# Kernel optimization log

Measured on AMD Instinct MI355X. Metric: run time of the kernel, lower is better.

Reference implementation:

```python
import jax, jax.numpy as jnp
import numpy as np

N_NODES = 50000


def _gcn_conv(x, W, b, src, dst, norm, n_nodes):
    # x: [N, Fin], W: [Fin, Fout]
    h = x @ W                                   # [N, Fout]
    msg = h[src] * norm[:, None]                # [E+N, Fout] edge messages
    out = jax.ops.segment_sum(msg, dst, num_segments=n_nodes)
    return out + b


def reference(x, edge_index, W1, b1, W2, b2):
    n = x.shape[0]
    # add self-loops (PyG GCNConv default add_self_loops=True)
    loop = jnp.arange(n, dtype=edge_index.dtype)
    src = jnp.concatenate([edge_index[0], loop])
    dst = jnp.concatenate([edge_index[1], loop])
    # symmetric degree normalization: deg over destination with unit weights
    deg = jax.ops.segment_sum(jnp.ones_like(dst, dtype=x.dtype), dst, num_segments=n)
    dinv = jnp.where(deg > 0, jax.lax.rsqrt(deg), 0.0)
    norm = dinv[src] * dinv[dst]                # [E+N]
    h = _gcn_conv(x, W1, b1, src, dst, norm, n)
    h = jax.nn.relu(h)
    out = _gcn_conv(h, W2, b2, src, dst, norm, n)
    return out


def setup_inputs() -> dict:
    key = jax.random.key(0)
    k1, k2, k3, k4 = jax.random.split(key, 4)
    n, e, fin, hid, fout = N_NODES, 800000, 128, 128, 64
    x = jax.random.normal(k1, (n, fin), dtype=jnp.float32)
    edge_index = jax.random.randint(k2, (2, e), 0, n, dtype=jnp.int64)
    # Glorot-ish init for linear weights, zero bias (PyG default)
    W1 = jax.random.normal(k3, (fin, hid), dtype=jnp.float32) / np.sqrt(fin)
    b1 = jnp.zeros((hid,), dtype=jnp.float32)
    W2 = jax.random.normal(k4, (hid, fout), dtype=jnp.float32) / np.sqrt(hid)
    b2 = jnp.zeros((fout,), dtype=jnp.float32)
    return {"x": x, "edge_index": edge_index, "W1": W1, "b1": b1, "W2": W2, "b2": b2}
```

## Files before the change

### kernel.cpp

```cpp
#include <hip/hip_runtime.h>
#include <hip/hip_bf16.h>


constexpr int FIN = 128;
constexpr int HID = 128;
constexpr int FOUT = 64;
constexpr int CAP = 48;
constexpr int OVF_MAX = 196608;

typedef __attribute__((ext_vector_type(8))) short s16x8;
typedef __attribute__((ext_vector_type(4))) float f32x4;

static __device__ __forceinline__ float bf2f(__hip_bfloat16 v) { return __bfloat162float(v); }
static __device__ __forceinline__ float lo2f(unsigned u) { union { unsigned i; float f; } c; c.i = u << 16; return c.f; }
static __device__ __forceinline__ float hi2f(unsigned u) { union { unsigned i; float f; } c; c.i = u & 0xffff0000u; return c.f; }
static __device__ __forceinline__ unsigned short f2bfu(float f) {
    __hip_bfloat16 h = __float2bfloat16(f);
    union { __hip_bfloat16 h; unsigned short u; } c; c.h = h; return c.u;
}
static __device__ __forceinline__ unsigned pack2(float a, float b) {
    return (unsigned)f2bfu(a) | ((unsigned)f2bfu(b) << 16);
}
static __device__ __forceinline__ void acc_add(float* acc, uint4 v) {
    acc[0] += lo2f(v.x); acc[1] += hi2f(v.x);
    acc[2] += lo2f(v.y); acc[3] += hi2f(v.y);
    acc[4] += lo2f(v.z); acc[5] += hi2f(v.z);
    acc[6] += lo2f(v.w); acc[7] += hi2f(v.w);
}

__global__ __launch_bounds__(256) void k_detect(const unsigned* __restrict__ xw,
                                                const int* __restrict__ eiw,
                                                int E, int* __restrict__ flags,
                                                int* __restrict__ cnt, int N) {
    for (long i = (long)blockIdx.x * 256 + threadIdx.x; i <= N; i += (long)gridDim.x * 256)
        cnt[i] = 0;
    if (blockIdx.x != 0) return;
    __shared__ int s_bf16like, s_oddnz;
    if (threadIdx.x == 0) { s_bf16like = 0; s_oddnz = 0; }
    __syncthreads();
    int c = 0;
    for (int i = threadIdx.x; i < 4096; i += 256) {
        unsigned ex = ((xw[i] & 0xffffu) >> 7) & 0xffu;
        if (ex >= 117u && ex <= 130u) c++;
    }
    atomicAdd(&s_bf16like, c);
    int nz = 0;
    for (int i = threadIdx.x; i < 2048; i += 256)
        if (eiw[2 * i + 1] != 0) nz++;
    atomicAdd(&s_oddnz, nz);
    __syncthreads();
    if (threadIdx.x == 0) {
        flags[0] = (s_bf16like < 2048) ? 1 : 0;
        flags[1] = (s_oddnz == 0) ? 1 : 0;
    }
}

__global__ __launch_bounds__(256) void k_build(const int* __restrict__ ei, int E, int N,
                                               int* __restrict__ cnt,
                                               int* __restrict__ slots,
                                               int* __restrict__ ovf,
                                               int* __restrict__ ovfcnt,
                                               const int* __restrict__ flags) {
    long i = (long)blockIdx.x * 256 + threadIdx.x;
    if (i >= E) return;
    int s, d;
    if (flags[1]) {
        s = ((const int2*)ei)[i].x;
        d = ((const int2*)(ei + 2 * (long)E))[i].x;
    } else {
        s = ei[i];
        d = ei[(long)E + i];
    }
    if ((unsigned)s >= (unsigned)N || (unsigned)d >= (unsigned)N) return;
    int pos = atomicAdd(&cnt[d], 1);
    if (pos < CAP) {
        slots[(long)d * CAP + pos] = s;
    } else {
        int op = atomicAdd(ovfcnt, 1);
        if (op < OVF_MAX) { ovf[2 * op] = d; ovf[2 * op + 1] = s; }
    }
}

template<int CT>
__global__ __launch_bounds__(256) void k_gemm(const void* __restrict__ Xp, int x_follows_flag,
                                              const void* __restrict__ Wp,
                                              const int* __restrict__ cnt,
                                              __hip_bfloat16* __restrict__ G,
                                              const int* __restrict__ flags, int N) {
    constexpr int C = CT * 16;
    __shared__ __align__(16) short Wt[C * 136];
    const bool f32m = flags[0] != 0;
    const bool xf32 = (x_follows_flag != 0) && f32m;
    const int tid = threadIdx.x;
    for (int i = tid; i < 128 * C; i += 256) {
        int k = i / C, n = i % C;
        float wv = f32m ? ((const float*)Wp)[(long)k * C + n]
                        : bf2f(((const __hip_bfloat16*)Wp)[(long)k * C + n]);
        Wt[n * 136 + k] = (short)f2bfu(wv);
    }
    __syncthreads();
    const int w = tid >> 6, lane = tid & 63;
    const int m = lane & 15, quad = lane >> 4;
    const int rowA = blockIdx.x * 64 + w * 16 + m;
    const int rowc = rowA < N ? rowA : N - 1;
    s16x8 afr[4];
#pragma unroll
    for (int kc = 0; kc < 4; ++kc) {
        const int k0 = kc * 32 + quad * 8;
        if (!xf32) {
            afr[kc] = *(const s16x8*)((const __hip_bfloat16*)Xp + (long)rowc * 128 + k0);
        } else {
            const float* p = (const float*)Xp + (long)rowc * 128 + k0;
            s16x8 t;
#pragma unroll
            for (int j = 0; j < 8; ++j) t[j] = (short)f2bfu(p[j]);
            afr[kc] = t;
        }
    }
    const int rbase = blockIdx.x * 64 + w * 16 + quad * 4;
    float dv[4];
#pragma unroll
    for (int r = 0; r < 4; ++r) {
        int rr = min(rbase + r, N - 1);
        dv[r] = rsqrtf((float)(cnt[rr] + 1));
    }
#pragma unroll
    for (int ct = 0; ct < CT; ++ct) {
        f32x4 acc = {0.f, 0.f, 0.f, 0.f};
#pragma unroll
        for (int kc = 0; kc < 4; ++kc) {
            s16x8 bfr = *(const s16x8*)&Wt[(ct * 16 + m) * 136 + kc * 32 + quad * 8];
            acc = __builtin_amdgcn_mfma_f32_16x16x32_bf16(afr[kc], bfr, acc, 0, 0, 0);
        }
#pragma unroll
        for (int r = 0; r < 4; ++r) {
            int rr = rbase + r;
            if (rr < N) G[(long)rr * C + ct * 16 + m] = __float2bfloat16(dv[r] * acc[r]);
        }
    }
}

template<int F, int LAYER1>
__global__ __launch_bounds__(256) void k_gather(const __hip_bfloat16* __restrict__ G,
                                                const int* __restrict__ cnt,
                                                const int* __restrict__ slots,
                                                const int* __restrict__ ovf,
                                                const int* __restrict__ ovfcnt,
                                                const void* __restrict__ bias,
                                                void* __restrict__ outp,
                                                const int* __restrict__ flags, int N) {
    constexpr int L = F / 8;
    constexpr int NODES = 256 / L;
    const int tid = threadIdx.x;
    const int grp = tid / L, lane = tid % L;
    const int node = blockIdx.x * NODES + grp;
    if (node >= N) return;
    const int cd = cnt[node];
    const float wself = rsqrtf((float)(cd + 1));
    const int m = cd < CAP ? cd : CAP;
    const int* sl = slots + (long)node * CAP;
    float acc[8] = {0, 0, 0, 0, 0, 0, 0, 0};
    acc_add(acc, ((const uint4*)(G + (long)node * F))[lane]);
    int i = 0;
    for (; i + 3 < m; i += 4) {
        int s0 = sl[i], s1 = sl[i + 1], s2 = sl[i + 2], s3 = sl[i + 3];
        uint4 v0 = ((const uint4*)(G + (long)s0 * F))[lane];
        uint4 v1 = ((const uint4*)(G + (long)s1 * F))[lane];
        uint4 v2 = ((const uint4*)(G + (long)s2 * F))[lane];
        uint4 v3 = ((const uint4*)(G + (long)s3 * F))[lane];
        acc_add(acc, v0); acc_add(acc, v1); acc_add(acc, v2); acc_add(acc, v3);
    }
    for (; i < m; ++i)
        acc_add(acc, ((const uint4*)(G + (long)sl[i] * F))[lane]);
    if (cd > CAP) {
        int oc = *ovfcnt; oc = oc < OVF_MAX ? oc : OVF_MAX;
        for (int j = 0; j < oc; ++j)
            if (ovf[2 * j] == node)
                acc_add(acc, ((const uint4*)(G + (long)ovf[2 * j + 1] * F))[lane]);
    }
    const bool f32m = flags[0] != 0;
    const int c0 = lane * 8;
    float bv[8];
    if (f32m) {
        const float4* bp = (const float4*)((const float*)bias + c0);
        float4 b0 = bp[0], b1 = bp[1];
        bv[0] = b0.x; bv[1] = b0.y; bv[2] = b0.z; bv[3] = b0.w;
        bv[4] = b1.x; bv[5] = b1.y; bv[6] = b1.z; bv[7] = b1.w;
    } else {
        uint4 b = *(const uint4*)((const __hip_bfloat16*)bias + c0);
        bv[0] = lo2f(b.x); bv[1] = hi2f(b.x); bv[2] = lo2f(b.y); bv[3] = hi2f(b.y);
        bv[4] = lo2f(b.z); bv[5] = hi2f(b.z); bv[6] = lo2f(b.w); bv[7] = hi2f(b.w);
    }
    float o[8];
#pragma unroll
    for (int c = 0; c < 8; ++c) {
        float v = wself * acc[c] + bv[c];
        o[c] = (LAYER1 && v < 0.f) ? 0.f : v;
    }
    if (LAYER1 || !f32m) {
        uint4 pv = { pack2(o[0], o[1]), pack2(o[2], o[3]), pack2(o[4], o[5]), pack2(o[6], o[7]) };
        ((uint4*)outp)[(long)node * L + lane] = pv;
    } else {
        float4* op = (float4*)((float*)outp + (long)node * F + c0);
        op[0] = make_float4(o[0], o[1], o[2], o[3]);
        op[1] = make_float4(o[4], o[5], o[6], o[7]);
    }
}

extern "C" void kernel_launch(void* const* d_in, const int* in_sizes, int n_in,
                              void* d_out, int out_size, void* d_ws, size_t ws_size,
                              hipStream_t stream) {
    const void* x  = d_in[0];
    const int*  ei = (const int*)d_in[1];
    const void* W1 = d_in[2];
    const void* b1 = d_in[3];
    const void* W2 = d_in[4];
    const void* b2 = d_in[5];

    const int N = in_sizes[0] / FIN;
    const int E = in_sizes[1] / 2;

    char* ws = (char*)d_ws;
    int*   flags  = (int*)ws;
    int*   cnt    = (int*)(ws + 4096);
    int*   ovfcnt = cnt + N;
    int*   ovf    = (int*)(ws + 524288);
    int*   slots  = (int*)(ws + 2097152);
    __hip_bfloat16* g  = (__hip_bfloat16*)(ws + 11730944);
    __hip_bfloat16* h1 = (__hip_bfloat16*)(ws + 24530944);
    __hip_bfloat16* g2 = (__hip_bfloat16*)(ws + 37330944);

    const int EB = (E + 255) / 256;
    const int GB = (N + 63) / 64;

    k_detect<<<64, 256, 0, stream>>>((const unsigned*)x, ei, E, flags, cnt, N);
    k_build<<<EB, 256, 0, stream>>>(ei, E, N, cnt, slots, ovf, ovfcnt, flags);
    k_gemm<8><<<GB, 256, 0, stream>>>(x, 1, W1, cnt, g, flags, N);
    k_gather<128, 1><<<(N + 15) / 16, 256, 0, stream>>>(g, cnt, slots, ovf, ovfcnt, b1, h1, flags, N);
    k_gemm<4><<<GB, 256, 0, stream>>>(h1, 0, W2, cnt, g2, flags, N);
    k_gather<64, 0><<<(N + 31) / 32, 256, 0, stream>>>(g2, cnt, slots, ovf, ovfcnt, b2, d_out, flags, N);
}
```

Measured before the change: 230.5 us.

## Build adjacency via two-pass bucketed binning in shared memory instead of global atomics

Replaces the single-pass adjacency build, which did one global atomic per edge on per-node counters, with a two-phase binning. First, edges are histogrammed per bucket of 98 destination nodes and scattered into bucket arrays using LDS atomics plus one global atomic per bucket per block. Then each bucket's slot table is assembled in shared memory and written out with coalesced vector stores. A patch kernel handles bucket overflow, and workspace buffers are reused (g2 aliases g, pairs aliases h1). This adds two kernel launches and more scratch traffic, and depends on the bucket capacity assumption holding.

```diff
diff --git a/kernel.cpp b/kernel.cpp
--- a/kernel.cpp
+++ b/kernel.cpp
@@ -6,7 +6,9 @@
 constexpr int HID = 128;
 constexpr int FOUT = 64;
 constexpr int CAP = 48;
-constexpr int OVF_MAX = 196608;
+constexpr int NPB = 98;
+constexpr int BCAP = 3072;
+constexpr int OVF_MAX = 65536;
 
 typedef __attribute__((ext_vector_type(8))) short s16x8;
 typedef __attribute__((ext_vector_type(4))) float f32x4;
@@ -31,10 +33,8 @@
 __global__ __launch_bounds__(256) void k_detect(const unsigned* __restrict__ xw,
                                                 const int* __restrict__ eiw,
                                                 int E, int* __restrict__ flags,
-                                                int* __restrict__ cnt, int N) {
-    for (long i = (long)blockIdx.x * 256 + threadIdx.x; i <= N; i += (long)gridDim.x * 256)
-        cnt[i] = 0;
-    if (blockIdx.x != 0) return;
+                                                int* __restrict__ gcur) {
+    for (int i = threadIdx.x; i < 1026; i += 256) gcur[i] = 0;
     __shared__ int s_bf16like, s_oddnz;
     if (threadIdx.x == 0) { s_bf16like = 0; s_oddnz = 0; }
     __syncthreads();
@@ -55,29 +55,106 @@
     }
 }
 
-__global__ __launch_bounds__(256) void k_build(const int* __restrict__ ei, int E, int N,
+__global__ __launch_bounds__(256) void k_binA(const int* __restrict__ ei, int E, int N,
+                                              int nbuk,
+                                              int* __restrict__ gcur,
+                                              int2* __restrict__ pairs,
+                                              int2* __restrict__ ovfA,
+                                              int* __restrict__ ovfAcnt,
+                                              const int* __restrict__ flags) {
+    __shared__ int hist[1024];
+    __shared__ int gbase[1024];
+    const int tid = threadIdx.x;
+    const long base = (long)blockIdx.x * 4096;
+    const bool i64 = flags[1] != 0;
+    for (int b = tid; b < nbuk; b += 256) hist[b] = 0;
+    __syncthreads();
+    for (int j = 0; j < 16; ++j) {
+        long i = base + j * 256 + tid;
+        if (i >= E) break;
+        int s, d;
+        if (i64) { s = ((const int2*)ei)[i].x; d = ((const int2*)(ei + 2 * (long)E))[i].x; }
+        else     { s = ei[i]; d = ei[(long)E + i]; }
+        if ((unsigned)s >= (unsigned)N || (unsigned)d >= (unsigned)N) continue;
+        atomicAdd(&hist[d / NPB], 1);
+    }
+    __syncthreads();
+    for (int b = tid; b < nbuk; b += 256) {
+        int h = hist[b];
+        gbase[b] = h > 0 ? atomicAdd(&gcur[b], h) : 0;
+        hist[b] = 0;
+    }
+    __syncthreads();
+    for (int j = 0; j < 16; ++j) {
+        long i = base + j * 256 + tid;
+        if (i >= E) break;
+        int s, d;
+        if (i64) { s = ((const int2*)ei)[i].x; d = ((const int2*)(ei + 2 * (long)E))[i].x; }
+        else     { s = ei[i]; d = ei[(long)E + i]; }
+        if ((unsigned)s >= (unsigned)N || (unsigned)d >= (unsigned)N) continue;
+        int b = d / NPB;
+        int p = gbase[b] + atomicAdd(&hist[b], 1);
+        if (p < BCAP) {
+            pairs[(long)b * BCAP + p] = make_int2(d, s);
+        } else {
+            int op = atomicAdd(ovfAcnt, 1);
+            if (op < OVF_MAX) ovfA[op] = make_int2(d, s);
+        }
+    }
+}
+
+__global__ __launch_bounds__(256) void k_binB(const int* __restrict__ gcur,
+                                              const int2* __restrict__ pairs,
+                                              int* __restrict__ cnt,
+                                              int* __restrict__ slots,
+                                              int2* __restrict__ ovf2,
+                                              int* __restrict__ ovf2cnt, int N) {
+    __shared__ int cntL[NPB];
+    __shared__ __align__(16) int slotsL[NPB * CAP];
+    const int b = blockIdx.x;
+    const int tid = threadIdx.x;
+    const int d0 = b * NPB;
+    const int nd = min(NPB, N - d0);
+    if (nd <= 0) return;
+    for (int i = tid; i < NPB; i += 256) cntL[i] = 0;
+    __syncthreads();
+    const int c = min(gcur[b], BCAP);
+    const int2* pb = pairs + (long)b * BCAP;
+    for (int i = tid; i < c; i += 256) {
+        int2 p = pb[i];
+        int ld = p.x - d0;
+        int pos = atomicAdd(&cntL[ld], 1);
+        if (pos < CAP) {
+            slotsL[ld * CAP + pos] = p.y;
+        } else {
+            int op = atomicAdd(ovf2cnt, 1);
+            if (op < OVF_MAX) ovf2[op] = p;
+        }
+    }
+    __syncthreads();
+    for (int i = tid; i < nd; i += 256) cnt[d0 + i] = cntL[i];
+    const uint4* sv = (const uint4*)slotsL;
+    uint4* gv = (uint4*)(slots + (long)d0 * CAP);
+    const int total4 = (nd * CAP) >> 2;
+    for (int i = tid; i < total4; i += 256) gv[i] = sv[i];
+}
+
+__global__ __launch_bounds__(256) void k_patch(const int2* __restrict__ ovfA,
+                                               const int* __restrict__ ovfAcnt,
                                                int* __restrict__ cnt,
                                                int* __restrict__ slots,
-                                               int* __restrict__ ovf,
-                                               int* __restrict__ ovfcnt,
-                                               const int* __restrict__ flags) {
-    long i = (long)blockIdx.x * 256 + threadIdx.x;
-    if (i >= E) return;
-    int s, d;
-    if (flags[1]) {
-        s = ((const int2*)ei)[i].x;
-        d = ((const int2*)(ei + 2 * (long)E))[i].x;
-    } else {
-        s = ei[i];
-        d = ei[(long)E + i];
-    }
-    if ((unsigned)s >= (unsigned)N || (unsigned)d >= (unsigned)N) return;
-    int pos = atomicAdd(&cnt[d], 1);
-    if (pos < CAP) {
-        slots[(long)d * CAP + pos] = s;
-    } else {
-        int op = atomicAdd(ovfcnt, 1);
-        if (op < OVF_MAX) { ovf[2 * op] = d; ovf[2 * op + 1] = s; }
+                                               int2* __restrict__ ovf2,
+                                               int* __restrict__ ovf2cnt, int N) {
+    int n = *ovfAcnt; n = n < OVF_MAX ? n : OVF_MAX;
+    for (int i = blockIdx.x * 256 + threadIdx.x; i < n; i += gridDim.x * 256) {
+        int2 p = ovfA[i];
+        int pos = atomicAdd(&cnt[p.x], 1);
+        if (pos < CAP) {
+            slots[(long)p.x * CAP + pos] = p.y;
+        } else {
+            int op = atomicAdd(ovf2cnt, 1);
+            if (op < OVF_MAX) ovf2[op] = p;
+        }
     }
 }
 
@@ -144,8 +221,8 @@
 __global__ __launch_bounds__(256) void k_gather(const __hip_bfloat16* __restrict__ G,
                                                 const int* __restrict__ cnt,
                                                 const int* __restrict__ slots,
-                                                const int* __restrict__ ovf,
-                                                const int* __restrict__ ovfcnt,
+                                                const int2* __restrict__ ovf2,
+                                                const int* __restrict__ ovf2cnt,
                                                 const void* __restrict__ bias,
                                                 void* __restrict__ outp,
                                                 const int* __restrict__ flags, int N) {
@@ -173,10 +250,10 @@
     for (; i < m; ++i)
         acc_add(acc, ((const uint4*)(G + (long)sl[i] * F))[lane]);
     if (cd > CAP) {
-        int oc = *ovfcnt; oc = oc < OVF_MAX ? oc : OVF_MAX;
+        int oc = *ovf2cnt; oc = oc < OVF_MAX ? oc : OVF_MAX;
         for (int j = 0; j < oc; ++j)
-            if (ovf[2 * j] == node)
-                acc_add(acc, ((const uint4*)(G + (long)ovf[2 * j + 1] * F))[lane]);
+            if (ovf2[j].x == node)
+                acc_add(acc, ((const uint4*)(G + (long)ovf2[j].y * F))[lane]);
     }
     const bool f32m = flags[0] != 0;
     const int c0 = lane * 8;
@@ -219,24 +296,31 @@
 
     const int N = in_sizes[0] / FIN;
     const int E = in_sizes[1] / 2;
+    const int nbuk = (N + NPB - 1) / NPB;
 
     char* ws = (char*)d_ws;
-    int*   flags  = (int*)ws;
-    int*   cnt    = (int*)(ws + 4096);
-    int*   ovfcnt = cnt + N;
-    int*   ovf    = (int*)(ws + 524288);
-    int*   slots  = (int*)(ws + 2097152);
+    int*   flags   = (int*)ws;
+    int*   gcur    = (int*)(ws + 4096);
+    int*   ovfAcnt = gcur + 1024;
+    int*   ovf2cnt = gcur + 1025;
+    int*   cnt     = (int*)(ws + 65536);
+    int2*  ovfA    = (int2*)(ws + 524288);
+    int2*  ovf2    = (int2*)(ws + 1048576);
+    int*   slots   = (int*)(ws + 2097152);
     __hip_bfloat16* g  = (__hip_bfloat16*)(ws + 11730944);
+    __hip_bfloat16* g2 = g;
+    int2*  pairs   = (int2*)(ws + 24530944);
     __hip_bfloat16* h1 = (__hip_bfloat16*)(ws + 24530944);
-    __hip_bfloat16* g2 = (__hip_bfloat16*)(ws + 37330944);
-
-    const int EB = (E + 255) / 256;
+
     const int GB = (N + 63) / 64;
-
-    k_detect<<<64, 256, 0, stream>>>((const unsigned*)x, ei, E, flags, cnt, N);
-    k_build<<<EB, 256, 0, stream>>>(ei, E, N, cnt, slots, ovf, ovfcnt, flags);
+    const int AB = (E + 4095) / 4096;
+
+    k_detect<<<1, 256, 0, stream>>>((const unsigned*)x, ei, E, flags, gcur);
+    k_binA<<<AB, 256, 0, stream>>>(ei, E, N, nbuk, gcur, pairs, ovfA, ovfAcnt, flags);
+    k_binB<<<nbuk, 256, 0, stream>>>(gcur, pairs, cnt, slots, ovf2, ovf2cnt, N);
+    k_patch<<<32, 256, 0, stream>>>(ovfA, ovfAcnt, cnt, slots, ovf2, ovf2cnt, N);
     k_gemm<8><<<GB, 256, 0, stream>>>(x, 1, W1, cnt, g, flags, N);
-    k_gather<128, 1><<<(N + 15) / 16, 256, 0, stream>>>(g, cnt, slots, ovf, ovfcnt, b1, h1, flags, N);
+    k_gather<128, 1><<<(N + 15) / 16, 256, 0, stream>>>(g, cnt, slots, ovf2, ovf2cnt, b1, h1, flags, N);
     k_gemm<4><<<GB, 256, 0, stream>>>(h1, 0, W2, cnt, g2, flags, N);
-    k_gather<64, 0><<<(N + 31) / 32, 256, 0, stream>>>(g2, cnt, slots, ovf, ovfcnt, b2, d_out, flags, N);
-}
+    k_gather<64, 0><<<(N + 31) / 32, 256, 0, stream>>>(g2, cnt, slots, ovf2, ovf2cnt, b2, d_out, flags, N);
+}
```

Measured after the change: 204.7 us. 11.2% less time.
